# Kernel optimization log

Hardware: AMD Instinct MI355X
Metric: run time of the kernel (lower is better)

The kernel has to match this reference:

```python
import jax, jax.numpy as jnp
import numpy as np

N_NODES = 20000
N_EDGES = 320000
IN_DIM = 256
OUT_DIM = 256
N_HEADS = 4
D_K = OUT_DIM // N_HEADS
N_NTYPES = 4
N_RELS = 8
SQRT_DK = float(np.sqrt(D_K))


def setup_inputs() -> dict:
    key = jax.random.key(0)
    ks = jax.random.split(key, 12)
    xav = lambda k, shape, fan: jax.random.normal(k, shape, jnp.float32) * (1.0 / np.sqrt(fan))
    return {
        "h": jax.random.normal(ks[0], (N_NODES, IN_DIM), jnp.float32),
        "k_linears": xav(ks[1], (N_NTYPES, IN_DIM, OUT_DIM), IN_DIM),
        "q_linears": xav(ks[2], (N_NTYPES, IN_DIM, OUT_DIM), IN_DIM),
        "v_linears": xav(ks[3], (N_NTYPES, IN_DIM, OUT_DIM), IN_DIM),
        "a_linears": xav(ks[4], (N_NTYPES, OUT_DIM, OUT_DIM), OUT_DIM),
        "relation_att": xav(ks[5], (N_RELS, N_HEADS, D_K, D_K), D_K),
        "relation_msg": xav(ks[6], (N_RELS, N_HEADS, D_K, D_K), D_K),
        "relation_pri": jnp.ones((N_RELS, N_HEADS), jnp.float32),
        "skip": jnp.ones((N_NTYPES,), jnp.float32),
        "node_type": jax.random.randint(ks[7], (N_NODES,), 0, N_NTYPES),
        "etype": jnp.sort(jax.random.randint(ks[8], (N_EDGES,), 0, N_RELS)),
        "row_idx": jax.random.randint(ks[9], (N_EDGES,), 0, N_NODES),
        "col_idx": jax.random.randint(ks[10], (N_EDGES,), 0, N_NODES),
    }


def _typed_matmul(x, W, node_type):
    # x: [N, in], W: [T, in, out] -> per-node-type projection [N, out]
    all_t = jnp.einsum("ni,tio->tno", x, W)  # [T, N, out]
    return all_t[node_type, jnp.arange(x.shape[0])]


def reference(h, k_linears, q_linears, v_linears, a_linears,
              relation_att, relation_msg, relation_pri, skip,
              node_type, etype, row_idx, col_idx):
    n = h.shape[0]
    # per-node-type K/Q/V projections -> [N, H, d_k]
    k = _typed_matmul(h, k_linears, node_type).reshape(n, N_HEADS, D_K)
    q = _typed_matmul(h, q_linears, node_type).reshape(n, N_HEADS, D_K)
    v = _typed_matmul(h, v_linears, node_type).reshape(n, N_HEADS, D_K)

    # per-relation transforms computed at node granularity, gathered per edge
    q_att = jnp.einsum("nhd,rhde->rnhe", q, relation_att)  # [R, N, H, d_k]
    v_msg = jnp.einsum("nhd,rhde->rnhe", v, relation_msg)  # [R, N, H, d_k]

    aw_q_edge = q_att[etype, col_idx]   # [E, H, d_k]  (dst-side q transformed by rel att)
    msg_edge = v_msg[etype, row_idx]    # [E, H, d_k]  (src-side v transformed by rel msg)

    # attention score: <rel_att @ q_dst, k_src> * pri_r / sqrt(d_k)  -> [E, H]
    attn_score = jnp.sum(aw_q_edge * k[row_idx], axis=-1)
    score = attn_score * (relation_pri[etype] / SQRT_DK)

    # edge softmax over incoming edges of each destination node
    m = jax.ops.segment_max(score, col_idx, num_segments=n)       # [N, H]
    ex = jnp.exp(score - m[col_idx])                              # [E, H]
    denom = jax.ops.segment_sum(ex, col_idx, num_segments=n)      # [N, H]
    alpha = ex / denom[col_idx]                                   # [E, H]

    agg = jax.ops.segment_sum(alpha[..., None] * msg_edge, col_idx,
                              num_segments=n)                     # [N, H, d_k]
    agg = agg.reshape(n, OUT_DIM)

    # output per-node-type projection scaled by sigmoid(skip[type])
    out = _typed_matmul(agg, a_linears, node_type)
    out = jax.nn.sigmoid(skip)[node_type][:, None] * out
    return out
```

## Files before the change

### kernel.cpp

```cpp
#include <hip/hip_runtime.h>

static constexpr int NN  = 20000;
static constexpr int NE  = 320000;
static constexpr int NTY = 4;
static constexpr int NRL = 8;
static constexpr int NB  = NRL * NN;

static constexpr int ZB = (NB + NN * 4 + 255) / 256;
static constexpr int WB = 4 * 768;
static constexpr int AB = 4 * 256;
static constexpr int RB = 32 * 4096 / 256;
static constexpr int CB = (NN + 255) / 256;

typedef short bf16x8 __attribute__((ext_vector_type(8)));
typedef float f32x4  __attribute__((ext_vector_type(4)));
typedef unsigned short u16x4 __attribute__((ext_vector_type(4)));

__device__ __forceinline__ unsigned short f2bf(float f) {
  unsigned u = __float_as_uint(f);
  u += 0x7fffu + ((u >> 16) & 1u);
  return (unsigned short)(u >> 16);
}
__device__ __forceinline__ float bf2f(unsigned short b) {
  return __uint_as_float(((unsigned)b) << 16);
}
__device__ __forceinline__ f32x4 mfma16(bf16x8 a, bf16x8 b, f32x4 c) {
  return __builtin_amdgcn_mfma_f32_16x16x32_bf16(a, b, c, 0, 0, 0);
}

__global__ void k_tcount(const int* __restrict__ ntype, int* __restrict__ c4p) {
  __shared__ int c[4];
  if (threadIdx.x < 4) c[threadIdx.x] = 0;
  __syncthreads();
  int i = blockIdx.x * 256 + threadIdx.x;
  if (i < NN) atomicAdd(&c[ntype[i]], 1);
  __syncthreads();
  if (threadIdx.x < 4) c4p[blockIdx.x * 4 + threadIdx.x] = c[threadIdx.x];
}
__global__ void k_meta(const int* __restrict__ c4p, int* toff, int* ncur,
                       int* mt64_t, int* mt64_m, int* gcnt) {
  __shared__ int c4[4];
  __shared__ int ts[5];
  if (threadIdx.x < 4) {
    int s = 0;
    for (int b = 0; b < CB; ++b) s += c4p[b * 4 + threadIdx.x];
    c4[threadIdx.x] = s;
  }
  __syncthreads();
  if (threadIdx.x == 0) {
    int s = 0, s2 = 0;
    for (int t = 0; t < NTY; ++t) {
      toff[t] = s; ncur[t] = s; s += c4[t];
      ts[t] = s2; s2 += (c4[t] + 63) >> 6;
    }
    toff[NTY] = s; ts[NTY] = s2; gcnt[0] = s2;
  }
  __syncthreads();
  int n64 = ts[4];
  for (int i = threadIdx.x; i < n64; i += 256) {
    int t = 0;
    while (t < 3 && i >= ts[t + 1]) ++t;
    mt64_t[i] = t; mt64_m[i] = i - ts[t];
  }
}
__global__ void k_nscatter(const int* __restrict__ key, int* cur,
                           int* nperm, int* inv) {
  int i = blockIdx.x * 256 + threadIdx.x;
  if (i < NN) {
    int p = atomicAdd(&cur[key[i]], 1);
    nperm[p] = i;
    inv[i] = p;
  }
}

__global__ void k_prep_all(const float* __restrict__ Wk,
                           const float* __restrict__ Wq, const float* __restrict__ Wv,
                           const float* __restrict__ Wa, const float* __restrict__ ratt,
                           const float* __restrict__ rmsg,
                           int* bcnt, float* denom,
                           unsigned short* Wt, unsigned short* At,
                           unsigned short* Att, unsigned short* Mt) {
  int b = blockIdx.x;
  if (b < ZB) {
    int i = b * 256 + threadIdx.x;
    if (i < NB) bcnt[i] = 0;
    else if (i < NB + NN * 4) denom[i - NB] = 0.f;
  } else if (b < ZB + WB) {
    int bb = b - ZB;
    int j = bb % 768, t = bb / 768, i = threadIdx.x;
    const float* src; int c;
    if (j < 256)      { src = Wk; c = j; }
    else if (j < 512) { src = Wq; c = j - 256; }
    else              { src = Wv; c = j - 512; }
    Wt[(t * 768 + j) * 256 + i] = f2bf(src[(t * 256 + i) * 256 + c]);
  } else if (b < ZB + WB + AB) {
    int bb = b - (ZB + WB);
    int j = bb % 256, t = bb / 256, i = threadIdx.x;
    At[(t * 256 + j) * 256 + i] = f2bf(Wa[(t * 256 + i) * 256 + j]);
  } else {
    int idx = (b - (ZB + WB + AB)) * 256 + threadIdx.x;
    int rh = idx >> 12, e = (idx >> 6) & 63, d = idx & 63;
    Att[idx] = f2bf(ratt[rh * 4096 + d * 64 + e]);
    Mt[idx]  = f2bf(rmsg[rh * 4096 + d * 64 + e]);
  }
}

__global__ void k_bcount(const int* __restrict__ etyp, const int* __restrict__ coli,
                         const int* __restrict__ inv, int* bcnt) {
  int e = blockIdx.x * 256 + threadIdx.x;
  if (e < NE) atomicAdd(&bcnt[etyp[e] * NN + inv[coli[e]]], 1);
}
__global__ void k_scan1(const int* cnt, int* off, int* psum) {
  __shared__ int sm[256];
  int i = blockIdx.x * 256 + threadIdx.x;
  int v = cnt[i];
  sm[threadIdx.x] = v;
  __syncthreads();
  for (int d = 1; d < 256; d <<= 1) {
    int t = (threadIdx.x >= d) ? sm[threadIdx.x - d] : 0;
    __syncthreads();
    sm[threadIdx.x] += t;
    __syncthreads();
  }
  off[i] = sm[threadIdx.x] - v;
  if (threadIdx.x == 255) psum[blockIdx.x] = sm[255];
}
__global__ void k_scan2(int* psum) {
  __shared__ int sm[1024];
  int t = threadIdx.x;
  int v = (t < 625) ? psum[t] : 0;
  sm[t] = v;
  __syncthreads();
  for (int d = 1; d < 1024; d <<= 1) {
    int x = (t >= d) ? sm[t - d] : 0;
    __syncthreads();
    sm[t] += x;
    __syncthreads();
  }
  if (t < 625) psum[t] = sm[t] - v;
}
__global__ void k_scan3(int* off, int* cur, const int* psum) {
  int i = blockIdx.x * 256 + threadIdx.x;
  int v = off[i] + psum[blockIdx.x];
  off[i] = v; cur[i] = v;
  if (i == 0) off[NB] = NE;
}
__global__ void k_escatter(const int* __restrict__ etyp, const int* __restrict__ rowi,
                           const int* __restrict__ coli, const int* __restrict__ inv,
                           int* cur, int* je) {
  int e = blockIdx.x * 256 + threadIdx.x;
  if (e >= NE) return;
  int bin = etyp[e] * NN + inv[coli[e]];
  int j = atomicAdd(&cur[bin], 1);
  je[j] = inv[rowi[e]];
}

__global__ __launch_bounds__(256) void k_gemm_kqv(
    const float* __restrict__ hsrc, const unsigned short* __restrict__ Wt,
    const int* __restrict__ nperm, const int* __restrict__ toff,
    const int* __restrict__ mt64_t, const int* __restrict__ mt64_m,
    const int* __restrict__ gcnt,
    unsigned short* __restrict__ kvb, unsigned short* __restrict__ qb) {
  __shared__ unsigned short bs[16][264];
  int mtile = blockIdx.x;
  if (mtile >= gcnt[0]) return;
  int wave = threadIdx.x >> 6, lane = threadIdx.x & 63;
  int t = mt64_t[mtile], tm = mt64_m[mtile];
  int base = toff[t], cnt = toff[t + 1] - base;
  int lr = lane & 15, kq = lane >> 4;
  int arow = tm * 64 + wave * 16 + lr;
  int prow = base + (arow < cnt ? arow : cnt - 1);
  int node = nperm[prow];
  const float* ap = hsrc + (size_t)node * 256 + kq * 8;
  bf16x8 af[8];
#pragma unroll
  for (int s = 0; s < 8; ++s) {
    f32x4 x0 = *(const f32x4*)(ap + s * 32);
    f32x4 x1 = *(const f32x4*)(ap + s * 32 + 4);
    bf16x8 o;
    o[0] = (short)f2bf(x0[0]); o[1] = (short)f2bf(x0[1]);
    o[2] = (short)f2bf(x0[2]); o[3] = (short)f2bf(x0[3]);
    o[4] = (short)f2bf(x1[0]); o[5] = (short)f2bf(x1[1]);
    o[6] = (short)f2bf(x1[2]); o[7] = (short)f2bf(x1[3]);
    af[s] = o;
  }
  int pr[4]; bool wr[4];
#pragma unroll
  for (int i = 0; i < 4; ++i) {
    int crow = tm * 64 + wave * 16 + kq * 4 + i;
    wr[i] = crow < cnt;
    pr[i] = base + (wr[i] ? crow : 0);
  }
  int sc = threadIdx.x >> 4;
  int seg = threadIdx.x & 15;
  for (int tn = 0; tn < 48; ++tn) {
    const unsigned short* wsrc = Wt + ((size_t)(t * 768 + tn * 16 + sc)) * 256 + seg * 16;
    __syncthreads();
    *(bf16x8*)&bs[sc][seg * 16]     = *(const bf16x8*)wsrc;
    *(bf16x8*)&bs[sc][seg * 16 + 8] = *(const bf16x8*)(wsrc + 8);
    __syncthreads();
    f32x4 acc = {0.f, 0.f, 0.f, 0.f};
#pragma unroll
    for (int s = 0; s < 8; ++s)
      acc = mfma16(af[s], *(const bf16x8*)&bs[lr][kq * 8 + s * 32], acc);
    int ccol = tn * 16 + lr;
#pragma unroll
    for (int i = 0; i < 4; ++i) {
      if (wr[i]) {
        unsigned short v = f2bf(acc[i]);
        if (ccol < 256)
          kvb[(size_t)pr[i] * 512 + (ccol >> 6) * 128 + (ccol & 63)] = v;
        else if (ccol < 512)
          qb[(size_t)pr[i] * 256 + (ccol - 256)] = v;
        else {
          int c = ccol - 512;
          kvb[(size_t)pr[i] * 512 + (c >> 6) * 128 + 64 + (c & 63)] = v;
        }
      }
    }
  }
}

__global__ __launch_bounds__(256) void k_mega(
    const int* __restrict__ boff, const int* __restrict__ je,
    const unsigned short* __restrict__ qb, const unsigned short* __restrict__ kvb,
    const unsigned short* __restrict__ Att, const unsigned short* __restrict__ Mt,
    const float* __restrict__ pri, unsigned short* __restrict__ aggh,
    float* __restrict__ denom) {
  __shared__ unsigned short qsh[4][32][80];
  int dt = blockIdx.x >> 2, quarter = blockIdx.x & 3;
  int h = threadIdx.x >> 6, lane = threadIdx.x & 63;
  int lr16 = lane & 15, kq4 = lane >> 4;
  int lr32 = lane & 31, kq1 = lane >> 5;
  int r0 = quarter * 2;
  float dtot = 0.f;
  f32x4 C[2][4] = {{{0.f,0.f,0.f,0.f},{0.f,0.f,0.f,0.f},{0.f,0.f,0.f,0.f},{0.f,0.f,0.f,0.f}},
                   {{0.f,0.f,0.f,0.f},{0.f,0.f,0.f,0.f},{0.f,0.f,0.f,0.f},{0.f,0.f,0.f,0.f}}};
  for (int rr = 0; rr < 2; ++rr) {
    int r = r0 + rr;
    int rh = r * 4 + h;
    int bin = r * NN + dt * 32 + lr32;
    int b0 = boff[bin], b1 = boff[bin + 1];
#pragma unroll
    for (int hf = 0; hf < 2; ++hf) {
      const unsigned short* ap = qb + (size_t)(dt * 32 + hf * 16 + lr16) * 256 + h * 64 + kq4 * 8;
      bf16x8 aq0 = *(const bf16x8*)ap;
      bf16x8 aq1 = *(const bf16x8*)(ap + 32);
#pragma unroll
      for (int tn = 0; tn < 4; ++tn) {
        const unsigned short* bp = Att + ((rh * 64 + tn * 16 + lr16) * 64) + kq4 * 8;
        f32x4 a = {0.f, 0.f, 0.f, 0.f};
        a = mfma16(aq0, *(const bf16x8*)bp, a);
        a = mfma16(aq1, *(const bf16x8*)(bp + 32), a);
#pragma unroll
        for (int i = 0; i < 4; ++i)
          qsh[h][hf * 16 + kq4 * 4 + i][tn * 16 + lr16] = f2bf(a[i]);
      }
    }
    bf16x8 qtp[4];
#pragma unroll
    for (int g = 0; g < 4; ++g)
      qtp[g] = *(const bf16x8*)&qsh[h][lr32][kq1 * 32 + g * 8];
    float acc[32];
#pragma unroll
    for (int m = 0; m < 32; ++m) acc[m] = 0.f;
    float prs = pri[rh] * 0.125f;
    for (int j = b0; j < b1; ++j) {
      int src = je[j];
      const unsigned short* kp = kvb + (size_t)src * 512 + h * 128 + kq1 * 32;
      bf16x8 k0 = *(const bf16x8*)kp;
      bf16x8 k1 = *(const bf16x8*)(kp + 8);
      bf16x8 k2 = *(const bf16x8*)(kp + 16);
      bf16x8 k3 = *(const bf16x8*)(kp + 24);
      bf16x8 v0 = *(const bf16x8*)(kp + 64);
      bf16x8 v1 = *(const bf16x8*)(kp + 72);
      bf16x8 v2 = *(const bf16x8*)(kp + 80);
      bf16x8 v3 = *(const bf16x8*)(kp + 88);
      float s = 0.f;
#pragma unroll
      for (int m = 0; m < 8; ++m) {
        s += bf2f((unsigned short)qtp[0][m]) * bf2f((unsigned short)k0[m]);
        s += bf2f((unsigned short)qtp[1][m]) * bf2f((unsigned short)k1[m]);
        s += bf2f((unsigned short)qtp[2][m]) * bf2f((unsigned short)k2[m]);
        s += bf2f((unsigned short)qtp[3][m]) * bf2f((unsigned short)k3[m]);
      }
      s += __shfl_xor(s, 32);
      float ex = __expf(s * prs);
      dtot += ex;
#pragma unroll
      for (int m = 0; m < 8; ++m) {
        acc[m]      += ex * bf2f((unsigned short)v0[m]);
        acc[8 + m]  += ex * bf2f((unsigned short)v1[m]);
        acc[16 + m] += ex * bf2f((unsigned short)v2[m]);
        acc[24 + m] += ex * bf2f((unsigned short)v3[m]);
      }
    }
#pragma unroll
    for (int g = 0; g < 4; ++g) {
      bf16x8 o;
#pragma unroll
      for (int m = 0; m < 8; ++m) o[m] = (short)f2bf(acc[g * 8 + m]);
      *(bf16x8*)&qsh[h][lr32][kq1 * 32 + g * 8] = o;
    }
#pragma unroll
    for (int hf = 0; hf < 2; ++hf) {
      bf16x8 m0 = *(const bf16x8*)&qsh[h][hf * 16 + lr16][kq4 * 8];
      bf16x8 m1 = *(const bf16x8*)&qsh[h][hf * 16 + lr16][32 + kq4 * 8];
#pragma unroll
      for (int tn = 0; tn < 4; ++tn) {
        const unsigned short* bp = Mt + ((rh * 64 + tn * 16 + lr16) * 64) + kq4 * 8;
        C[hf][tn] = mfma16(m0, *(const bf16x8*)bp, C[hf][tn]);
        C[hf][tn] = mfma16(m1, *(const bf16x8*)(bp + 32), C[hf][tn]);
      }
    }
  }
  if (kq1 == 0) atomicAdd(&denom[(dt * 32 + lr32) * 4 + h], dtot);
#pragma unroll
  for (int hf = 0; hf < 2; ++hf)
#pragma unroll
    for (int tn = 0; tn < 4; ++tn)
#pragma unroll
      for (int i = 0; i < 4; ++i)
        aggh[((size_t)quarter * NN + dt * 32 + hf * 16 + kq4 * 4 + i) * 256 +
             h * 64 + tn * 16 + lr16] = f2bf(C[hf][tn][i]);
}

__global__ __launch_bounds__(256) void k_gemm_out(
    const unsigned short* __restrict__ aggh, const float* __restrict__ denom,
    const unsigned short* __restrict__ At,
    const int* __restrict__ nperm, const int* __restrict__ toff,
    const int* __restrict__ mt64_t, const int* __restrict__ mt64_m,
    const int* __restrict__ gcnt,
    const float* __restrict__ skip, float* __restrict__ out) {
  __shared__ unsigned short bs[16][264];
  int mtile = blockIdx.x;
  if (mtile >= gcnt[0]) return;
  int wave = threadIdx.x >> 6, lane = threadIdx.x & 63;
  int t = mt64_t[mtile], tm = mt64_m[mtile];
  int base = toff[t], cnt = toff[t + 1] - base;
  int lr = lane & 15, kq = lane >> 4;
  int arow = tm * 64 + wave * 16 + lr;
  int prow = base + (arow < cnt ? arow : cnt - 1);
  float dn[4];
#pragma unroll
  for (int hh = 0; hh < 4; ++hh) {
    float d = denom[prow * 4 + hh];
    dn[hh] = d > 0.f ? 1.f / d : 0.f;
  }
  const unsigned short* g = aggh + (size_t)prow * 256 + kq * 8;
  bf16x8 af[8];
#pragma unroll
  for (int s = 0; s < 8; ++s) {
    bf16x8 x0 = *(const bf16x8*)(g + s * 32);
    bf16x8 x1 = *(const bf16x8*)(g + (size_t)NN * 256 + s * 32);
    bf16x8 x2 = *(const bf16x8*)(g + (size_t)2 * NN * 256 + s * 32);
    bf16x8 x3 = *(const bf16x8*)(g + (size_t)3 * NN * 256 + s * 32);
    float dv = dn[(kq * 8 + s * 32) >> 6];
#pragma unroll
    for (int m = 0; m < 8; ++m)
      af[s][m] = (short)f2bf((bf2f((unsigned short)x0[m]) + bf2f((unsigned short)x1[m]) +
                              bf2f((unsigned short)x2[m]) + bf2f((unsigned short)x3[m])) * dv);
  }
  int nd[4]; bool wr[4];
#pragma unroll
  for (int i = 0; i < 4; ++i) {
    int crow = tm * 64 + wave * 16 + kq * 4 + i;
    wr[i] = crow < cnt;
    nd[i] = nperm[base + (wr[i] ? crow : 0)];
  }
  float sg = 1.f / (1.f + __expf(-skip[t]));
  int sc = threadIdx.x >> 4;
  int seg = threadIdx.x & 15;
  for (int tn = 0; tn < 16; ++tn) {
    const unsigned short* wsrc = At + ((size_t)(t * 256 + tn * 16 + sc)) * 256 + seg * 16;
    __syncthreads();
    *(bf16x8*)&bs[sc][seg * 16]     = *(const bf16x8*)wsrc;
    *(bf16x8*)&bs[sc][seg * 16 + 8] = *(const bf16x8*)(wsrc + 8);
    __syncthreads();
    f32x4 acc = {0.f, 0.f, 0.f, 0.f};
#pragma unroll
    for (int s = 0; s < 8; ++s)
      acc = mfma16(af[s], *(const bf16x8*)&bs[lr][kq * 8 + s * 32], acc);
    int ccol = tn * 16 + lr;
#pragma unroll
    for (int i = 0; i < 4; ++i)
      if (wr[i]) out[nd[i] * 256 + ccol] = acc[i] * sg;
  }
}

extern "C" void kernel_launch(void* const* d_in, const int* in_sizes, int n_in,
                              void* d_out, int out_size, void* d_ws, size_t ws_size,
                              hipStream_t stream) {
  (void)in_sizes; (void)n_in; (void)out_size; (void)ws_size;
  const float* h    = (const float*)d_in[0];
  const float* Wk   = (const float*)d_in[1];
  const float* Wq   = (const float*)d_in[2];
  const float* Wv   = (const float*)d_in[3];
  const float* Wa   = (const float*)d_in[4];
  const float* ratt = (const float*)d_in[5];
  const float* rmsg = (const float*)d_in[6];
  const float* pri  = (const float*)d_in[7];
  const float* skp  = (const float*)d_in[8];
  const int* ntype  = (const int*)d_in[9];
  const int* etyp   = (const int*)d_in[10];
  const int* rowi   = (const int*)d_in[11];
  const int* coli   = (const int*)d_in[12];
  float* out = (float*)d_out;

  char* p = (char*)d_ws;
  auto alloc = [&](size_t bytes) {
    void* q = (void*)p;
    p += (bytes + 255) & ~(size_t)255;
    return q;
  };
  unsigned short* Wt   = (unsigned short*)alloc((size_t)4 * 768 * 256 * 2);
  unsigned short* At   = (unsigned short*)alloc((size_t)4 * 256 * 256 * 2);
  unsigned short* Att  = (unsigned short*)alloc((size_t)32 * 4096 * 2);
  unsigned short* Mt   = (unsigned short*)alloc((size_t)32 * 4096 * 2);
  unsigned short* kvb  = (unsigned short*)alloc((size_t)NN * 512 * 2);
  unsigned short* qb   = (unsigned short*)alloc((size_t)NN * 256 * 2);
  unsigned short* aggh = (unsigned short*)alloc((size_t)4 * NN * 256 * 2);
  float* denom = (float*)alloc((size_t)NN * 4 * 4);
  int* toff   = (int*)alloc(32);
  int* ncur   = (int*)alloc(16);
  int* c4p    = (int*)alloc((size_t)CB * 4 * 4);
  int* nperm  = (int*)alloc((size_t)NN * 4);
  int* inv    = (int*)alloc((size_t)NN * 4);
  int* bcnt   = (int*)alloc((size_t)NB * 4);
  int* boff   = (int*)alloc((size_t)(NB + 1) * 4);
  int* bcur   = (int*)alloc((size_t)NB * 4);
  int* psum   = (int*)alloc((size_t)625 * 4);
  int* je     = (int*)alloc((size_t)NE * 4);
  int* mt64_t = (int*)alloc((size_t)324 * 4);
  int* mt64_m = (int*)alloc((size_t)324 * 4);
  int* gcnt   = (int*)alloc(32);

  k_tcount<<<CB, 256, 0, stream>>>(ntype, c4p);
  k_meta<<<1, 256, 0, stream>>>(c4p, toff, ncur, mt64_t, mt64_m, gcnt);
  k_nscatter<<<CB, 256, 0, stream>>>(ntype, ncur, nperm, inv);

  k_prep_all<<<ZB + WB + AB + RB, 256, 0, stream>>>(
      Wk, Wq, Wv, Wa, ratt, rmsg, bcnt, denom, Wt, At, Att, Mt);

  k_bcount<<<(NE + 255) / 256, 256, 0, stream>>>(etyp, coli, inv, bcnt);
  k_scan1<<<625, 256, 0, stream>>>(bcnt, boff, psum);
  k_scan2<<<1, 1024, 0, stream>>>(psum);
  k_scan3<<<625, 256, 0, stream>>>(boff, bcur, psum);
  k_escatter<<<(NE + 255) / 256, 256, 0, stream>>>(etyp, rowi, coli, inv, bcur, je);

  k_gemm_kqv<<<320, 256, 0, stream>>>(h, Wt, nperm, toff, mt64_t, mt64_m, gcnt, kvb, qb);
  k_mega<<<2500, 256, 0, stream>>>(boff, je, qb, kvb, Att, Mt, pri, aggh, denom);
  k_gemm_out<<<320, 256, 0, stream>>>(aggh, denom, At, nperm, toff, mt64_t, mt64_m, gcnt,
                                      skp, out);
}
```

Measured before the change: 376.4 us.

## Split GEMM column tiles across more blocks and keep q/agg in fp32 smem

Both projection GEMMs now split their output columns across extra blocks: three chunks for the KQV GEMM and two for the output GEMM. This raises the block count from 320 on a large-CU GPU, at the cost of reloading and reconverting the A rows in every chunk. In the attention kernel the relation-transformed q and the aggregated messages are staged in shared memory as fp32 instead of bf16, which removes one rounding step but doubles LDS use per block. The kernel also prefetches the next edge's source index one iteration ahead to shorten the dependent load chain.

After: 337.2 us. 1.12x faster.

```diff
diff --git a/kernel.cpp b/kernel.cpp
--- a/kernel.cpp
+++ b/kernel.cpp
@@ -162,7 +162,7 @@
     const int* __restrict__ gcnt,
     unsigned short* __restrict__ kvb, unsigned short* __restrict__ qb) {
   __shared__ unsigned short bs[16][264];
-  int mtile = blockIdx.x;
+  int mtile = blockIdx.x / 3, chunk = blockIdx.x % 3;
   if (mtile >= gcnt[0]) return;
   int wave = threadIdx.x >> 6, lane = threadIdx.x & 63;
   int t = mt64_t[mtile], tm = mt64_m[mtile];
@@ -193,7 +193,8 @@
   }
   int sc = threadIdx.x >> 4;
   int seg = threadIdx.x & 15;
-  for (int tn = 0; tn < 48; ++tn) {
+  for (int tt = 0; tt < 16; ++tt) {
+    int tn = chunk * 16 + tt;
     const unsigned short* wsrc = Wt + ((size_t)(t * 768 + tn * 16 + sc)) * 256 + seg * 16;
     __syncthreads();
     *(bf16x8*)&bs[sc][seg * 16]     = *(const bf16x8*)wsrc;
@@ -227,7 +228,7 @@
     const unsigned short* __restrict__ Att, const unsigned short* __restrict__ Mt,
     const float* __restrict__ pri, unsigned short* __restrict__ aggh,
     float* __restrict__ denom) {
-  __shared__ unsigned short qsh[4][32][80];
+  __shared__ float qsh[4][32][68];
   int dt = blockIdx.x >> 2, quarter = blockIdx.x & 3;
   int h = threadIdx.x >> 6, lane = threadIdx.x & 63;
   int lr16 = lane & 15, kq4 = lane >> 4;
@@ -254,19 +255,23 @@
         a = mfma16(aq1, *(const bf16x8*)(bp + 32), a);
 #pragma unroll
         for (int i = 0; i < 4; ++i)
-          qsh[h][hf * 16 + kq4 * 4 + i][tn * 16 + lr16] = f2bf(a[i]);
-      }
-    }
-    bf16x8 qtp[4];
-#pragma unroll
-    for (int g = 0; g < 4; ++g)
-      qtp[g] = *(const bf16x8*)&qsh[h][lr32][kq1 * 32 + g * 8];
+          qsh[h][hf * 16 + kq4 * 4 + i][tn * 16 + lr16] = a[i];
+      }
+    }
+    float qt[32];
+#pragma unroll
+    for (int m = 0; m < 32; m += 4) {
+      f32x4 v = *(const f32x4*)&qsh[h][lr32][kq1 * 32 + m];
+      qt[m] = v[0]; qt[m + 1] = v[1]; qt[m + 2] = v[2]; qt[m + 3] = v[3];
+    }
     float acc[32];
 #pragma unroll
     for (int m = 0; m < 32; ++m) acc[m] = 0.f;
     float prs = pri[rh] * 0.125f;
+    int src_next = (b0 < b1) ? je[b0] : 0;
     for (int j = b0; j < b1; ++j) {
-      int src = je[j];
+      int src = src_next;
+      if (j + 1 < b1) src_next = je[j + 1];
       const unsigned short* kp = kvb + (size_t)src * 512 + h * 128 + kq1 * 32;
       bf16x8 k0 = *(const bf16x8*)kp;
       bf16x8 k1 = *(const bf16x8*)(kp + 8);
@@ -279,10 +284,10 @@
       float s = 0.f;
 #pragma unroll
       for (int m = 0; m < 8; ++m) {
-        s += bf2f((unsigned short)qtp[0][m]) * bf2f((unsigned short)k0[m]);
-        s += bf2f((unsigned short)qtp[1][m]) * bf2f((unsigned short)k1[m]);
-        s += bf2f((unsigned short)qtp[2][m]) * bf2f((unsigned short)k2[m]);
-        s += bf2f((unsigned short)qtp[3][m]) * bf2f((unsigned short)k3[m]);
+        s += qt[m]      * bf2f((unsigned short)k0[m]);
+        s += qt[8 + m]  * bf2f((unsigned short)k1[m]);
+        s += qt[16 + m] * bf2f((unsigned short)k2[m]);
+        s += qt[24 + m] * bf2f((unsigned short)k3[m]);
       }
       s += __shfl_xor(s, 32);
       float ex = __expf(s * prs);
@@ -296,16 +301,18 @@
       }
     }
 #pragma unroll
-    for (int g = 0; g < 4; ++g) {
-      bf16x8 o;
-#pragma unroll
-      for (int m = 0; m < 8; ++m) o[m] = (short)f2bf(acc[g * 8 + m]);
-      *(bf16x8*)&qsh[h][lr32][kq1 * 32 + g * 8] = o;
+    for (int m = 0; m < 32; m += 4) {
+      f32x4 v = {acc[m], acc[m + 1], acc[m + 2], acc[m + 3]};
+      *(f32x4*)&qsh[h][lr32][kq1 * 32 + m] = v;
     }
 #pragma unroll
     for (int hf = 0; hf < 2; ++hf) {
-      bf16x8 m0 = *(const bf16x8*)&qsh[h][hf * 16 + lr16][kq4 * 8];
-      bf16x8 m1 = *(const bf16x8*)&qsh[h][hf * 16 + lr16][32 + kq4 * 8];
+      bf16x8 m0, m1;
+#pragma unroll
+      for (int m = 0; m < 8; ++m) {
+        m0[m] = (short)f2bf(qsh[h][hf * 16 + lr16][kq4 * 8 + m]);
+        m1[m] = (short)f2bf(qsh[h][hf * 16 + lr16][32 + kq4 * 8 + m]);
+      }
 #pragma unroll
       for (int tn = 0; tn < 4; ++tn) {
         const unsigned short* bp = Mt + ((rh * 64 + tn * 16 + lr16) * 64) + kq4 * 8;
@@ -333,7 +340,7 @@
     const int* __restrict__ gcnt,
     const float* __restrict__ skip, float* __restrict__ out) {
   __shared__ unsigned short bs[16][264];
-  int mtile = blockIdx.x;
+  int mtile = blockIdx.x >> 1, chunk = blockIdx.x & 1;
   if (mtile >= gcnt[0]) return;
   int wave = threadIdx.x >> 6, lane = threadIdx.x & 63;
   int t = mt64_t[mtile], tm = mt64_m[mtile];
@@ -371,7 +378,8 @@
   float sg = 1.f / (1.f + __expf(-skip[t]));
   int sc = threadIdx.x >> 4;
   int seg = threadIdx.x & 15;
-  for (int tn = 0; tn < 16; ++tn) {
+  for (int tt = 0; tt < 8; ++tt) {
+    int tn = chunk * 8 + tt;
     const unsigned short* wsrc = At + ((size_t)(t * 256 + tn * 16 + sc)) * 256 + seg * 16;
     __syncthreads();
     *(bf16x8*)&bs[sc][seg * 16]     = *(const bf16x8*)wsrc;
@@ -448,8 +456,8 @@
   k_scan3<<<625, 256, 0, stream>>>(boff, bcur, psum);
   k_escatter<<<(NE + 255) / 256, 256, 0, stream>>>(etyp, rowi, coli, inv, bcur, je);
 
-  k_gemm_kqv<<<320, 256, 0, stream>>>(h, Wt, nperm, toff, mt64_t, mt64_m, gcnt, kvb, qb);
+  k_gemm_kqv<<<960, 256, 0, stream>>>(h, Wt, nperm, toff, mt64_t, mt64_m, gcnt, kvb, qb);
   k_mega<<<2500, 256, 0, stream>>>(boff, je, qb, kvb, Att, Mt, pri, aggh, denom);
-  k_gemm_out<<<320, 256, 0, stream>>>(aggh, denom, At, nperm, toff, mt64_t, mt64_m, gcnt,
+  k_gemm_out<<<640, 256, 0, stream>>>(aggh, denom, At, nperm, toff, mt64_t, mt64_m, gcnt,
                                       skp, out);
 }
```
